# Performance work log

Hardware: AMD Instinct MI355X
Metric: run time of the kernel (lower is better)

The kernel has to match this reference:

```python
import jax, jax.numpy as jnp
import numpy as np

N_NODES = 100000
N_EDGES = 1600000
IN_FEATS = 128
OUT_FEATS = 128


def setup_inputs() -> dict:
    key = jax.random.key(0)
    ks = jax.random.split(key, 8)
    feat = jax.random.normal(ks[0], (N_NODES, IN_FEATS), dtype=jnp.float32)
    weight = jax.random.normal(ks[1], (IN_FEATS, OUT_FEATS), dtype=jnp.float32) * (1.0 / np.sqrt(IN_FEATS))
    bias = jnp.zeros((OUT_FEATS,), dtype=jnp.float32)
    s = 1.0 / np.sqrt(OUT_FEATS)
    w_ih = jax.random.uniform(ks[2], (3 * OUT_FEATS, IN_FEATS), dtype=jnp.float32, minval=-s, maxval=s)
    w_hh = jax.random.uniform(ks[3], (3 * OUT_FEATS, OUT_FEATS), dtype=jnp.float32, minval=-s, maxval=s)
    b_ih = jax.random.uniform(ks[4], (3 * OUT_FEATS,), dtype=jnp.float32, minval=-s, maxval=s)
    b_hh = jax.random.uniform(ks[5], (3 * OUT_FEATS,), dtype=jnp.float32, minval=-s, maxval=s)
    src = jax.random.randint(ks[6], (N_EDGES,), 0, N_NODES, dtype=jnp.int32)
    dst = jax.random.randint(ks[7], (N_EDGES,), 0, N_NODES, dtype=jnp.int32)
    return {"feat": feat, "weight": weight, "bias": bias,
            "w_ih": w_ih, "w_hh": w_hh, "b_ih": b_ih, "b_hh": b_hh,
            "src": src, "dst": dst}


def reference(feat, weight, bias, w_ih, w_hh, b_ih, b_hh, src, dst):
    n = feat.shape[0]
    # symmetric-ish GCN norm: in-degree^{-1/2}, clamped at 1
    deg = jax.ops.segment_sum(jnp.ones(dst.shape, feat.dtype), dst, num_segments=n)
    norm = jnp.power(jnp.clip(deg, 1.0, None), -0.5)[:, None]  # [N,1]
    featn = feat * norm
    # copy_src + sum aggregation (SpMM via gather + segment_sum), then matmul
    agg = jax.ops.segment_sum(featn[src], dst, num_segments=n)  # [N, in]
    rst = agg @ weight                                           # [N, out]
    rst = rst * norm + bias
    # GRUCell(input=featn, hidden=rst)
    gi = featn @ w_ih.T + b_ih   # [N, 3*out]
    gh = rst @ w_hh.T + b_hh     # [N, 3*out]
    i_r, i_z, i_n = jnp.split(gi, 3, axis=1)
    h_r, h_z, h_n = jnp.split(gh, 3, axis=1)
    r = jax.nn.sigmoid(i_r + h_r)
    z = jax.nn.sigmoid(i_z + h_z)
    nn_ = jnp.tanh(i_n + r * h_n)
    return (1.0 - z) * nn_ + z * rst
```

## Files before the change

### kernel.cpp

```cpp
#include <hip/hip_runtime.h>
#include <hip/hip_bf16.h>
#include <math.h>

#define N_NODES 100000
#define N_EDGES 1600000
#define F 128


#define WS_FEATN_OFF 8001536
#define WS_WTI_OFF   59201536
#define WS_WTH_OFF   59398144
#define WS_NEED_FULL (WS_WTH_OFF + 196608)

__global__ __launch_bounds__(256) void k_degree(const int* __restrict__ dst,
                                                int* __restrict__ deg) {
    int i = blockIdx.x * 256 + threadIdx.x;
    if (i < N_EDGES) atomicAdd(&deg[dst[i]], 1);
}

#define SCAN_B 512
#define SCAN_NB 196

__global__ __launch_bounds__(SCAN_B) void k_scan1(const int* __restrict__ deg,
                                                  int* __restrict__ bsum) {
    __shared__ int s[SCAN_B];
    int t = threadIdx.x;
    int i = blockIdx.x * SCAN_B + t;
    s[t] = (i < N_NODES) ? deg[i] : 0;
    __syncthreads();
    for (int o = SCAN_B / 2; o > 0; o >>= 1) {
        if (t < o) s[t] += s[t + o];
        __syncthreads();
    }
    if (t == 0) bsum[blockIdx.x] = s[0];
}

__global__ __launch_bounds__(256) void k_scan2(int* __restrict__ bsum) {
    __shared__ int s[256];
    int t = threadIdx.x;
    int v = (t < SCAN_NB) ? bsum[t] : 0;
    s[t] = v;
    __syncthreads();
    for (int o = 1; o < 256; o <<= 1) {
        int x = (t >= o) ? s[t - o] : 0;
        __syncthreads();
        s[t] += x;
        __syncthreads();
    }
    if (t < SCAN_NB) bsum[t] = (t == 0) ? 0 : s[t - 1];
}

__global__ __launch_bounds__(SCAN_B) void k_scan3(const int* __restrict__ deg,
                                                  const int* __restrict__ bsum,
                                                  int* __restrict__ offs,
                                                  float* __restrict__ norm) {
    __shared__ int s[SCAN_B];
    int t = threadIdx.x;
    int i = blockIdx.x * SCAN_B + t;
    int v = (i < N_NODES) ? deg[i] : 0;
    s[t] = v;
    __syncthreads();
    for (int o = 1; o < SCAN_B; o <<= 1) {
        int x = (t >= o) ? s[t - o] : 0;
        __syncthreads();
        s[t] += x;
        __syncthreads();
    }
    if (i < N_NODES) {
        offs[i] = bsum[blockIdx.x] + s[t] - v;
        norm[i] = rsqrtf(fmaxf((float)v, 1.0f));
    }
    if (blockIdx.x == 0 && t == 0) offs[N_NODES] = N_EDGES;
}

__global__ __launch_bounds__(256) void k_fill(const int* __restrict__ src,
                                              const int* __restrict__ dst,
                                              const int* __restrict__ offs,
                                              int* __restrict__ cursor,
                                              int* __restrict__ ssrc) {
    int i = blockIdx.x * 256 + threadIdx.x;
    if (i < N_EDGES) {
        int d = dst[i];
        int p = atomicAdd(&cursor[d], 1);
        ssrc[offs[d] + p] = src[i];
    }
}

__global__ __launch_bounds__(256) void k_featn(const float* __restrict__ feat,
                                               const float* __restrict__ norm,
                                               float* __restrict__ featn) {
    int idx = blockIdx.x * 256 + threadIdx.x;
    int row = idx >> 5;
    float nv = norm[row];
    float4 v = ((const float4*)feat)[idx];
    v.x *= nv; v.y *= nv; v.z *= nv; v.w *= nv;
    ((float4*)featn)[idx] = v;
}

__global__ __launch_bounds__(256) void k_wt(const float* __restrict__ w,
                                            float* __restrict__ wT) {
    __shared__ float tile[32][33];
    int rt = blockIdx.x >> 2, ct = blockIdx.x & 3;
    int r0 = rt * 32, c0 = ct * 32;
    int tr = threadIdx.x >> 5, tc = threadIdx.x & 31;
#pragma unroll
    for (int i = 0; i < 32; i += 8)
        tile[tr + i][tc] = w[(r0 + tr + i) * 128 + c0 + tc];
    __syncthreads();
#pragma unroll
    for (int i = 0; i < 32; i += 8)
        wT[(c0 + tr + i) * 384 + r0 + tc] = tile[tc][tr + i];
}

#define ROWS 16
template <bool PRE>
__global__ __launch_bounds__(256) void k_fused(
    const float* __restrict__ fsrc, const float* __restrict__ norm,
    const int* __restrict__ offs, const int* __restrict__ ssrc,
    const float* __restrict__ W, const float* __restrict__ bias,
    const float* __restrict__ wih_, const float* __restrict__ whh_,
    const float* __restrict__ b_ih, const float* __restrict__ b_hh,
    float* __restrict__ out) {
    __shared__ float sagg[ROWS][F];
    __shared__ float sfeat[ROWS][F];
    __shared__ float srst[ROWS][F];
    __shared__ float snorm[ROWS];

    int t = threadIdx.x;
    int row0 = blockIdx.x * ROWS;

    if (t < ROWS) snorm[t] = norm[row0 + t];
    for (int i = t; i < ROWS * (F / 4); i += 256) {
        int r = i >> 5, c = i & 31;
        float4 f = ((const float4*)(fsrc + (size_t)(row0 + r) * F))[c];
        if (!PRE) {
            float nv = norm[row0 + r];
            f.x *= nv; f.y *= nv; f.z *= nv; f.w *= nv;
        }
        ((float4*)&sfeat[r][0])[c] = f;
    }

    int wave = t >> 6, lane = t & 63;
    int hf = lane >> 5, sub = lane & 31;
    for (int ln = wave; ln < ROWS; ln += 4) {
        int node = row0 + ln;
        int beg = offs[node], end = offs[node + 1];
        float4 acc = make_float4(0.f, 0.f, 0.f, 0.f);
        int e = beg;
        for (; e + 7 < end; e += 8) {
            int s0 = ssrc[e + 0 + hf];
            int s1 = ssrc[e + 2 + hf];
            int s2 = ssrc[e + 4 + hf];
            int s3 = ssrc[e + 6 + hf];
            float4 v0 = *(const float4*)(fsrc + (size_t)s0 * F + sub * 4);
            float4 v1 = *(const float4*)(fsrc + (size_t)s1 * F + sub * 4);
            float4 v2 = *(const float4*)(fsrc + (size_t)s2 * F + sub * 4);
            float4 v3 = *(const float4*)(fsrc + (size_t)s3 * F + sub * 4);
            if (PRE) {
                acc.x += (v0.x + v1.x) + (v2.x + v3.x);
                acc.y += (v0.y + v1.y) + (v2.y + v3.y);
                acc.z += (v0.z + v1.z) + (v2.z + v3.z);
                acc.w += (v0.w + v1.w) + (v2.w + v3.w);
            } else {
                float n0 = norm[s0], n1 = norm[s1], n2 = norm[s2], n3 = norm[s3];
                acc.x = fmaf(v0.x, n0, acc.x); acc.y = fmaf(v0.y, n0, acc.y);
                acc.z = fmaf(v0.z, n0, acc.z); acc.w = fmaf(v0.w, n0, acc.w);
                acc.x = fmaf(v1.x, n1, acc.x); acc.y = fmaf(v1.y, n1, acc.y);
                acc.z = fmaf(v1.z, n1, acc.z); acc.w = fmaf(v1.w, n1, acc.w);
                acc.x = fmaf(v2.x, n2, acc.x); acc.y = fmaf(v2.y, n2, acc.y);
                acc.z = fmaf(v2.z, n2, acc.z); acc.w = fmaf(v2.w, n2, acc.w);
                acc.x = fmaf(v3.x, n3, acc.x); acc.y = fmaf(v3.y, n3, acc.y);
                acc.z = fmaf(v3.z, n3, acc.z); acc.w = fmaf(v3.w, n3, acc.w);
            }
        }
        for (; e < end; e += 2) {
            int edge = e + hf;
            if (edge < end) {
                int s0 = ssrc[edge];
                float4 v0 = *(const float4*)(fsrc + (size_t)s0 * F + sub * 4);
                float n0 = PRE ? 1.0f : norm[s0];
                acc.x = fmaf(v0.x, n0, acc.x); acc.y = fmaf(v0.y, n0, acc.y);
                acc.z = fmaf(v0.z, n0, acc.z); acc.w = fmaf(v0.w, n0, acc.w);
            }
        }
        acc.x += __shfl_xor(acc.x, 32, 64);
        acc.y += __shfl_xor(acc.y, 32, 64);
        acc.z += __shfl_xor(acc.z, 32, 64);
        acc.w += __shfl_xor(acc.w, 32, 64);
        if (hf == 0) *(float4*)&sagg[ln][sub * 4] = acc;
    }
    __syncthreads();

    int j = t & 127;
    int rg = (t >> 7) * 8;
    {
        float acc[8] = {0, 0, 0, 0, 0, 0, 0, 0};
        for (int k = 0; k < F; k += 4) {
            float w0 = W[(k + 0) * F + j];
            float w1 = W[(k + 1) * F + j];
            float w2 = W[(k + 2) * F + j];
            float w3 = W[(k + 3) * F + j];
#pragma unroll
            for (int r = 0; r < 8; ++r) {
                float4 a = *(const float4*)&sagg[rg + r][k];
                acc[r] = fmaf(a.x, w0, acc[r]);
                acc[r] = fmaf(a.y, w1, acc[r]);
                acc[r] = fmaf(a.z, w2, acc[r]);
                acc[r] = fmaf(a.w, w3, acc[r]);
            }
        }
        float bj = bias[j];
#pragma unroll
        for (int r = 0; r < 8; ++r) {
            srst[rg + r][j] = acc[r] * snorm[rg + r] + bj;
        }
    }
    __syncthreads();

    float air[8] = {0}, aiz[8] = {0}, ain[8] = {0};
    float ahr[8] = {0}, ahz[8] = {0}, ahn[8] = {0};

    if (PRE) {
        for (int k = 0; k < F; k += 4) {
            float wi[3][4], wh[3][4];
#pragma unroll
            for (int kk = 0; kk < 4; ++kk) {
                const float* wik = wih_ + (size_t)(k + kk) * 384 + j;
                const float* whk = whh_ + (size_t)(k + kk) * 384 + j;
                wi[0][kk] = wik[0];   wi[1][kk] = wik[128]; wi[2][kk] = wik[256];
                wh[0][kk] = whk[0];   wh[1][kk] = whk[128]; wh[2][kk] = whk[256];
            }
#pragma unroll
            for (int r = 0; r < 8; ++r) {
                float4 a = *(const float4*)&sfeat[rg + r][k];
                float4 h = *(const float4*)&srst[rg + r][k];
                air[r] = fmaf(a.x, wi[0][0], air[r]); air[r] = fmaf(a.y, wi[0][1], air[r]);
                air[r] = fmaf(a.z, wi[0][2], air[r]); air[r] = fmaf(a.w, wi[0][3], air[r]);
                aiz[r] = fmaf(a.x, wi[1][0], aiz[r]); aiz[r] = fmaf(a.y, wi[1][1], aiz[r]);
                aiz[r] = fmaf(a.z, wi[1][2], aiz[r]); aiz[r] = fmaf(a.w, wi[1][3], aiz[r]);
                ain[r] = fmaf(a.x, wi[2][0], ain[r]); ain[r] = fmaf(a.y, wi[2][1], ain[r]);
                ain[r] = fmaf(a.z, wi[2][2], ain[r]); ain[r] = fmaf(a.w, wi[2][3], ain[r]);
                ahr[r] = fmaf(h.x, wh[0][0], ahr[r]); ahr[r] = fmaf(h.y, wh[0][1], ahr[r]);
                ahr[r] = fmaf(h.z, wh[0][2], ahr[r]); ahr[r] = fmaf(h.w, wh[0][3], ahr[r]);
                ahz[r] = fmaf(h.x, wh[1][0], ahz[r]); ahz[r] = fmaf(h.y, wh[1][1], ahz[r]);
                ahz[r] = fmaf(h.z, wh[1][2], ahz[r]); ahz[r] = fmaf(h.w, wh[1][3], ahz[r]);
                ahn[r] = fmaf(h.x, wh[2][0], ahn[r]); ahn[r] = fmaf(h.y, wh[2][1], ahn[r]);
                ahn[r] = fmaf(h.z, wh[2][2], ahn[r]); ahn[r] = fmaf(h.w, wh[2][3], ahn[r]);
            }
        }
    } else {
        const float* wir = wih_ + (size_t)(j + 0) * F;
        const float* wiz = wih_ + (size_t)(j + 128) * F;
        const float* win = wih_ + (size_t)(j + 256) * F;
        const float* whr = whh_ + (size_t)(j + 0) * F;
        const float* whz = whh_ + (size_t)(j + 128) * F;
        const float* whn = whh_ + (size_t)(j + 256) * F;
        for (int k = 0; k < F; k += 4) {
            float4 bir = *(const float4*)(wir + k);
            float4 biz = *(const float4*)(wiz + k);
            float4 bin = *(const float4*)(win + k);
            float4 bhr = *(const float4*)(whr + k);
            float4 bhz = *(const float4*)(whz + k);
            float4 bhn = *(const float4*)(whn + k);
#pragma unroll
            for (int r = 0; r < 8; ++r) {
                float4 a = *(const float4*)&sfeat[rg + r][k];
                float4 h = *(const float4*)&srst[rg + r][k];
                air[r] = fmaf(a.x, bir.x, air[r]); air[r] = fmaf(a.y, bir.y, air[r]);
                air[r] = fmaf(a.z, bir.z, air[r]); air[r] = fmaf(a.w, bir.w, air[r]);
                aiz[r] = fmaf(a.x, biz.x, aiz[r]); aiz[r] = fmaf(a.y, biz.y, aiz[r]);
                aiz[r] = fmaf(a.z, biz.z, aiz[r]); aiz[r] = fmaf(a.w, biz.w, aiz[r]);
                ain[r] = fmaf(a.x, bin.x, ain[r]); ain[r] = fmaf(a.y, bin.y, ain[r]);
                ain[r] = fmaf(a.z, bin.z, ain[r]); ain[r] = fmaf(a.w, bin.w, ain[r]);
                ahr[r] = fmaf(h.x, bhr.x, ahr[r]); ahr[r] = fmaf(h.y, bhr.y, ahr[r]);
                ahr[r] = fmaf(h.z, bhr.z, ahr[r]); ahr[r] = fmaf(h.w, bhr.w, ahr[r]);
                ahz[r] = fmaf(h.x, bhz.x, ahz[r]); ahz[r] = fmaf(h.y, bhz.y, ahz[r]);
                ahz[r] = fmaf(h.z, bhz.z, ahz[r]); ahz[r] = fmaf(h.w, bhz.w, ahz[r]);
                ahn[r] = fmaf(h.x, bhn.x, ahn[r]); ahn[r] = fmaf(h.y, bhn.y, ahn[r]);
                ahn[r] = fmaf(h.z, bhn.z, ahn[r]); ahn[r] = fmaf(h.w, bhn.w, ahn[r]);
            }
        }
    }

    float Bir = b_ih[j], Biz = b_ih[j + 128], Bin = b_ih[j + 256];
    float Bhr = b_hh[j], Bhz = b_hh[j + 128], Bhn = b_hh[j + 256];
#pragma unroll
    for (int r = 0; r < 8; ++r) {
        int row = row0 + rg + r;
        float ir = air[r] + Bir, hr = ahr[r] + Bhr;
        float iz = aiz[r] + Biz, hz = ahz[r] + Bhz;
        float in_ = ain[r] + Bin, hn = ahn[r] + Bhn;
        float rr = 1.0f / (1.0f + __expf(-(ir + hr)));
        float zz = 1.0f / (1.0f + __expf(-(iz + hz)));
        float nn = tanhf(in_ + rr * hn);
        float rstv = srst[rg + r][j];
        out[(size_t)row * F + j] = (1.0f - zz) * nn + zz * rstv;
    }
}

extern "C" void kernel_launch(void* const* d_in, const int* in_sizes, int n_in,
                              void* d_out, int out_size, void* d_ws, size_t ws_size,
                              hipStream_t stream) {
    const float* feat   = (const float*)d_in[0];
    const float* weight = (const float*)d_in[1];
    const float* bias   = (const float*)d_in[2];
    const float* w_ih   = (const float*)d_in[3];
    const float* w_hh   = (const float*)d_in[4];
    const float* b_ih   = (const float*)d_in[5];
    const float* b_hh   = (const float*)d_in[6];
    const int*   src    = (const int*)d_in[7];
    const int*   dst    = (const int*)d_in[8];
    float* out = (float*)d_out;

    char* ws = (char*)d_ws;
    int*   deg    = (int*)(ws + 0);
    float* norm   = (float*)(ws + 400000);
    int*   offs   = (int*)(ws + 800000);
    int*   cursor = (int*)(ws + 1200016);
    int*   ssrc   = (int*)(ws + 1600016);
    int*   bsum   = (int*)(ws + 8000016);
    float* featn  = (float*)(ws + WS_FEATN_OFF);
    float* wT_ih  = (float*)(ws + WS_WTI_OFF);
    float* wT_hh  = (float*)(ws + WS_WTH_OFF);

    hipMemsetAsync(deg, 0, N_NODES * sizeof(int), stream);
    hipMemsetAsync(cursor, 0, N_NODES * sizeof(int), stream);

    k_degree<<<(N_EDGES + 255) / 256, 256, 0, stream>>>(dst, deg);
    k_scan1<<<SCAN_NB, SCAN_B, 0, stream>>>(deg, bsum);
    k_scan2<<<1, 256, 0, stream>>>(bsum);
    k_scan3<<<SCAN_NB, SCAN_B, 0, stream>>>(deg, bsum, offs, norm);
    k_fill<<<(N_EDGES + 255) / 256, 256, 0, stream>>>(src, dst, offs, cursor, ssrc);

    if (ws_size >= WS_NEED_FULL) {
        k_wt<<<48, 256, 0, stream>>>(w_ih, wT_ih);
        k_wt<<<48, 256, 0, stream>>>(w_hh, wT_hh);
        k_featn<<<(N_NODES * F / 4) / 256, 256, 0, stream>>>(feat, norm, featn);
        k_fused<true><<<N_NODES / ROWS, 256, 0, stream>>>(featn, norm, offs, ssrc,
                                                          weight, bias, wT_ih, wT_hh,
                                                          b_ih, b_hh, out);
    } else {
        k_fused<false><<<N_NODES / ROWS, 256, 0, stream>>>(feat, norm, offs, ssrc,
                                                           weight, bias, w_ih, w_hh,
                                                           b_ih, b_hh, out);
    }
}
```

Measured before the change: 738.1 us.

## Halve fused-kernel row tile, merge GRU accumulators, fold launches and memset

Halves the rows per block in the fused aggregation+GRU kernel from 16 to 8 and adds a launch-bounds occupancy hint. It also merges the r/z input and hidden accumulators so 4 accumulator arrays are kept instead of 6 and bias loads are folded. The goal is lower register pressure and more resident waves for the latency-bound gather. Separately, the cursor memset moves into the scan kernel and the two weight-transpose launches become one, cutting launch overhead. The cost is that each block now reloads W and the GRU weights for half as many rows, doubling weight traffic from cache per output row.

New measurement: 830.6 us. 1.13x slower.

```diff
diff --git a/kernel.cpp b/kernel.cpp
--- a/kernel.cpp
+++ b/kernel.cpp
@@ -53,7 +53,8 @@
 __global__ __launch_bounds__(SCAN_B) void k_scan3(const int* __restrict__ deg,
                                                   const int* __restrict__ bsum,
                                                   int* __restrict__ offs,
-                                                  float* __restrict__ norm) {
+                                                  float* __restrict__ norm,
+                                                  int* __restrict__ cursor) {
     __shared__ int s[SCAN_B];
     int t = threadIdx.x;
     int i = blockIdx.x * SCAN_B + t;
@@ -69,6 +70,7 @@
     if (i < N_NODES) {
         offs[i] = bsum[blockIdx.x] + s[t] - v;
         norm[i] = rsqrtf(fmaxf((float)v, 1.0f));
+        cursor[i] = 0;
     }
     if (blockIdx.x == 0 && t == 0) offs[N_NODES] = N_EDGES;
 }
@@ -97,10 +99,16 @@
     ((float4*)featn)[idx] = v;
 }
 
-__global__ __launch_bounds__(256) void k_wt(const float* __restrict__ w,
-                                            float* __restrict__ wT) {
+__global__ __launch_bounds__(256) void k_wt(const float* __restrict__ w_ih,
+                                            const float* __restrict__ w_hh,
+                                            float* __restrict__ wT_ih,
+                                            float* __restrict__ wT_hh) {
     __shared__ float tile[32][33];
-    int rt = blockIdx.x >> 2, ct = blockIdx.x & 3;
+    int b = blockIdx.x;
+    const float* w = (b < 48) ? w_ih : w_hh;
+    float* wT      = (b < 48) ? wT_ih : wT_hh;
+    int bb = (b < 48) ? b : b - 48;
+    int rt = bb >> 2, ct = bb & 3;
     int r0 = rt * 32, c0 = ct * 32;
     int tr = threadIdx.x >> 5, tc = threadIdx.x & 31;
 #pragma unroll
@@ -112,9 +120,9 @@
         wT[(c0 + tr + i) * 384 + r0 + tc] = tile[tc][tr + i];
 }
 
-#define ROWS 16
+#define ROWS 8
 template <bool PRE>
-__global__ __launch_bounds__(256) void k_fused(
+__global__ __launch_bounds__(256, 4) void k_fused(
     const float* __restrict__ fsrc, const float* __restrict__ norm,
     const int* __restrict__ offs, const int* __restrict__ ssrc,
     const float* __restrict__ W, const float* __restrict__ bias,
@@ -130,8 +138,8 @@
     int row0 = blockIdx.x * ROWS;
 
     if (t < ROWS) snorm[t] = norm[row0 + t];
-    for (int i = t; i < ROWS * (F / 4); i += 256) {
-        int r = i >> 5, c = i & 31;
+    {
+        int r = t >> 5, c = t & 31;
         float4 f = ((const float4*)(fsrc + (size_t)(row0 + r) * F))[c];
         if (!PRE) {
             float nv = norm[row0 + r];
@@ -192,16 +200,16 @@
     __syncthreads();
 
     int j = t & 127;
-    int rg = (t >> 7) * 8;
+    int rg = (t >> 7) * 4;
     {
-        float acc[8] = {0, 0, 0, 0, 0, 0, 0, 0};
+        float acc[4] = {0, 0, 0, 0};
         for (int k = 0; k < F; k += 4) {
             float w0 = W[(k + 0) * F + j];
             float w1 = W[(k + 1) * F + j];
             float w2 = W[(k + 2) * F + j];
             float w3 = W[(k + 3) * F + j];
 #pragma unroll
-            for (int r = 0; r < 8; ++r) {
+            for (int r = 0; r < 4; ++r) {
                 float4 a = *(const float4*)&sagg[rg + r][k];
                 acc[r] = fmaf(a.x, w0, acc[r]);
                 acc[r] = fmaf(a.y, w1, acc[r]);
@@ -211,88 +219,88 @@
         }
         float bj = bias[j];
 #pragma unroll
-        for (int r = 0; r < 8; ++r) {
+        for (int r = 0; r < 4; ++r) {
             srst[rg + r][j] = acc[r] * snorm[rg + r] + bj;
         }
     }
     __syncthreads();
 
-    float air[8] = {0}, aiz[8] = {0}, ain[8] = {0};
-    float ahr[8] = {0}, ahz[8] = {0}, ahn[8] = {0};
+    float accr[4] = {0, 0, 0, 0};
+    float accz[4] = {0, 0, 0, 0};
+    float accin[4] = {0, 0, 0, 0};
+    float acchn[4] = {0, 0, 0, 0};
 
     if (PRE) {
         for (int k = 0; k < F; k += 4) {
-            float wi[3][4], wh[3][4];
+            float wir[4], wiz[4], win[4], whr[4], whz[4], whn[4];
 #pragma unroll
             for (int kk = 0; kk < 4; ++kk) {
                 const float* wik = wih_ + (size_t)(k + kk) * 384 + j;
                 const float* whk = whh_ + (size_t)(k + kk) * 384 + j;
-                wi[0][kk] = wik[0];   wi[1][kk] = wik[128]; wi[2][kk] = wik[256];
-                wh[0][kk] = whk[0];   wh[1][kk] = whk[128]; wh[2][kk] = whk[256];
-            }
-#pragma unroll
-            for (int r = 0; r < 8; ++r) {
+                wir[kk] = wik[0]; wiz[kk] = wik[128]; win[kk] = wik[256];
+                whr[kk] = whk[0]; whz[kk] = whk[128]; whn[kk] = whk[256];
+            }
+#pragma unroll
+            for (int r = 0; r < 4; ++r) {
                 float4 a = *(const float4*)&sfeat[rg + r][k];
                 float4 h = *(const float4*)&srst[rg + r][k];
-                air[r] = fmaf(a.x, wi[0][0], air[r]); air[r] = fmaf(a.y, wi[0][1], air[r]);
-                air[r] = fmaf(a.z, wi[0][2], air[r]); air[r] = fmaf(a.w, wi[0][3], air[r]);
-                aiz[r] = fmaf(a.x, wi[1][0], aiz[r]); aiz[r] = fmaf(a.y, wi[1][1], aiz[r]);
-                aiz[r] = fmaf(a.z, wi[1][2], aiz[r]); aiz[r] = fmaf(a.w, wi[1][3], aiz[r]);
-                ain[r] = fmaf(a.x, wi[2][0], ain[r]); ain[r] = fmaf(a.y, wi[2][1], ain[r]);
-                ain[r] = fmaf(a.z, wi[2][2], ain[r]); ain[r] = fmaf(a.w, wi[2][3], ain[r]);
-                ahr[r] = fmaf(h.x, wh[0][0], ahr[r]); ahr[r] = fmaf(h.y, wh[0][1], ahr[r]);
-                ahr[r] = fmaf(h.z, wh[0][2], ahr[r]); ahr[r] = fmaf(h.w, wh[0][3], ahr[r]);
-                ahz[r] = fmaf(h.x, wh[1][0], ahz[r]); ahz[r] = fmaf(h.y, wh[1][1], ahz[r]);
-                ahz[r] = fmaf(h.z, wh[1][2], ahz[r]); ahz[r] = fmaf(h.w, wh[1][3], ahz[r]);
-                ahn[r] = fmaf(h.x, wh[2][0], ahn[r]); ahn[r] = fmaf(h.y, wh[2][1], ahn[r]);
-                ahn[r] = fmaf(h.z, wh[2][2], ahn[r]); ahn[r] = fmaf(h.w, wh[2][3], ahn[r]);
+                accr[r] = fmaf(a.x, wir[0], accr[r]); accr[r] = fmaf(h.x, whr[0], accr[r]);
+                accr[r] = fmaf(a.y, wir[1], accr[r]); accr[r] = fmaf(h.y, whr[1], accr[r]);
+                accr[r] = fmaf(a.z, wir[2], accr[r]); accr[r] = fmaf(h.z, whr[2], accr[r]);
+                accr[r] = fmaf(a.w, wir[3], accr[r]); accr[r] = fmaf(h.w, whr[3], accr[r]);
+                accz[r] = fmaf(a.x, wiz[0], accz[r]); accz[r] = fmaf(h.x, whz[0], accz[r]);
+                accz[r] = fmaf(a.y, wiz[1], accz[r]); accz[r] = fmaf(h.y, whz[1], accz[r]);
+                accz[r] = fmaf(a.z, wiz[2], accz[r]); accz[r] = fmaf(h.z, whz[2], accz[r]);
+                accz[r] = fmaf(a.w, wiz[3], accz[r]); accz[r] = fmaf(h.w, whz[3], accz[r]);
+                accin[r] = fmaf(a.x, win[0], accin[r]); accin[r] = fmaf(a.y, win[1], accin[r]);
+                accin[r] = fmaf(a.z, win[2], accin[r]); accin[r] = fmaf(a.w, win[3], accin[r]);
+                acchn[r] = fmaf(h.x, whn[0], acchn[r]); acchn[r] = fmaf(h.y, whn[1], acchn[r]);
+                acchn[r] = fmaf(h.z, whn[2], acchn[r]); acchn[r] = fmaf(h.w, whn[3], acchn[r]);
             }
         }
     } else {
-        const float* wir = wih_ + (size_t)(j + 0) * F;
-        const float* wiz = wih_ + (size_t)(j + 128) * F;
-        const float* win = wih_ + (size_t)(j + 256) * F;
-        const float* whr = whh_ + (size_t)(j + 0) * F;
-        const float* whz = whh_ + (size_t)(j + 128) * F;
-        const float* whn = whh_ + (size_t)(j + 256) * F;
+        const float* wirp = wih_ + (size_t)(j + 0) * F;
+        const float* wizp = wih_ + (size_t)(j + 128) * F;
+        const float* winp = wih_ + (size_t)(j + 256) * F;
+        const float* whrp = whh_ + (size_t)(j + 0) * F;
+        const float* whzp = whh_ + (size_t)(j + 128) * F;
+        const float* whnp = whh_ + (size_t)(j + 256) * F;
         for (int k = 0; k < F; k += 4) {
-            float4 bir = *(const float4*)(wir + k);
-            float4 biz = *(const float4*)(wiz + k);
-            float4 bin = *(const float4*)(win + k);
-            float4 bhr = *(const float4*)(whr + k);
-            float4 bhz = *(const float4*)(whz + k);
-            float4 bhn = *(const float4*)(whn + k);
-#pragma unroll
-            for (int r = 0; r < 8; ++r) {
+            float4 bir = *(const float4*)(wirp + k);
+            float4 biz = *(const float4*)(wizp + k);
+            float4 bin = *(const float4*)(winp + k);
+            float4 bhr = *(const float4*)(whrp + k);
+            float4 bhz = *(const float4*)(whzp + k);
+            float4 bhn = *(const float4*)(whnp + k);
+#pragma unroll
+            for (int r = 0; r < 4; ++r) {
                 float4 a = *(const float4*)&sfeat[rg + r][k];
                 float4 h = *(const float4*)&srst[rg + r][k];
-                air[r] = fmaf(a.x, bir.x, air[r]); air[r] = fmaf(a.y, bir.y, air[r]);
-                air[r] = fmaf(a.z, bir.z, air[r]); air[r] = fmaf(a.w, bir.w, air[r]);
-                aiz[r] = fmaf(a.x, biz.x, aiz[r]); aiz[r] = fmaf(a.y, biz.y, aiz[r]);
-                aiz[r] = fmaf(a.z, biz.z, aiz[r]); aiz[r] = fmaf(a.w, biz.w, aiz[r]);
-                ain[r] = fmaf(a.x, bin.x, ain[r]); ain[r] = fmaf(a.y, bin.y, ain[r]);
-                ain[r] = fmaf(a.z, bin.z, ain[r]); ain[r] = fmaf(a.w, bin.w, ain[r]);
-                ahr[r] = fmaf(h.x, bhr.x, ahr[r]); ahr[r] = fmaf(h.y, bhr.y, ahr[r]);
-                ahr[r] = fmaf(h.z, bhr.z, ahr[r]); ahr[r] = fmaf(h.w, bhr.w, ahr[r]);
-                ahz[r] = fmaf(h.x, bhz.x, ahz[r]); ahz[r] = fmaf(h.y, bhz.y, ahz[r]);
-                ahz[r] = fmaf(h.z, bhz.z, ahz[r]); ahz[r] = fmaf(h.w, bhz.w, ahz[r]);
-                ahn[r] = fmaf(h.x, bhn.x, ahn[r]); ahn[r] = fmaf(h.y, bhn.y, ahn[r]);
-                ahn[r] = fmaf(h.z, bhn.z, ahn[r]); ahn[r] = fmaf(h.w, bhn.w, ahn[r]);
-            }
-        }
-    }
-
-    float Bir = b_ih[j], Biz = b_ih[j + 128], Bin = b_ih[j + 256];
-    float Bhr = b_hh[j], Bhz = b_hh[j + 128], Bhn = b_hh[j + 256];
-#pragma unroll
-    for (int r = 0; r < 8; ++r) {
+                accr[r] = fmaf(a.x, bir.x, accr[r]); accr[r] = fmaf(h.x, bhr.x, accr[r]);
+                accr[r] = fmaf(a.y, bir.y, accr[r]); accr[r] = fmaf(h.y, bhr.y, accr[r]);
+                accr[r] = fmaf(a.z, bir.z, accr[r]); accr[r] = fmaf(h.z, bhr.z, accr[r]);
+                accr[r] = fmaf(a.w, bir.w, accr[r]); accr[r] = fmaf(h.w, bhr.w, accr[r]);
+                accz[r] = fmaf(a.x, biz.x, accz[r]); accz[r] = fmaf(h.x, bhz.x, accz[r]);
+                accz[r] = fmaf(a.y, biz.y, accz[r]); accz[r] = fmaf(h.y, bhz.y, accz[r]);
+                accz[r] = fmaf(a.z, biz.z, accz[r]); accz[r] = fmaf(h.z, bhz.z, accz[r]);
+                accz[r] = fmaf(a.w, biz.w, accz[r]); accz[r] = fmaf(h.w, bhz.w, accz[r]);
+                accin[r] = fmaf(a.x, bin.x, accin[r]); accin[r] = fmaf(a.y, bin.y, accin[r]);
+                accin[r] = fmaf(a.z, bin.z, accin[r]); accin[r] = fmaf(a.w, bin.w, accin[r]);
+                acchn[r] = fmaf(h.x, bhn.x, acchn[r]); acchn[r] = fmaf(h.y, bhn.y, acchn[r]);
+                acchn[r] = fmaf(h.z, bhn.z, acchn[r]); acchn[r] = fmaf(h.w, bhn.w, acchn[r]);
+            }
+        }
+    }
+
+    float Brz = b_ih[j] + b_hh[j];
+    float Bzz = b_ih[j + 128] + b_hh[j + 128];
+    float Bin = b_ih[j + 256], Bhn = b_hh[j + 256];
+#pragma unroll
+    for (int r = 0; r < 4; ++r) {
         int row = row0 + rg + r;
-        float ir = air[r] + Bir, hr = ahr[r] + Bhr;
-        float iz = aiz[r] + Biz, hz = ahz[r] + Bhz;
-        float in_ = ain[r] + Bin, hn = ahn[r] + Bhn;
-        float rr = 1.0f / (1.0f + __expf(-(ir + hr)));
-        float zz = 1.0f / (1.0f + __expf(-(iz + hz)));
-        float nn = tanhf(in_ + rr * hn);
+        float rr = 1.0f / (1.0f + __expf(-(accr[r] + Brz)));
+        float zz = 1.0f / (1.0f + __expf(-(accz[r] + Bzz)));
+        float nn = tanhf(accin[r] + Bin + rr * (acchn[r] + Bhn));
         float rstv = srst[rg + r][j];
         out[(size_t)row * F + j] = (1.0f - zz) * nn + zz * rstv;
     }
@@ -324,17 +332,15 @@
     float* wT_hh  = (float*)(ws + WS_WTH_OFF);
 
     hipMemsetAsync(deg, 0, N_NODES * sizeof(int), stream);
-    hipMemsetAsync(cursor, 0, N_NODES * sizeof(int), stream);
 
     k_degree<<<(N_EDGES + 255) / 256, 256, 0, stream>>>(dst, deg);
     k_scan1<<<SCAN_NB, SCAN_B, 0, stream>>>(deg, bsum);
     k_scan2<<<1, 256, 0, stream>>>(bsum);
-    k_scan3<<<SCAN_NB, SCAN_B, 0, stream>>>(deg, bsum, offs, norm);
+    k_scan3<<<SCAN_NB, SCAN_B, 0, stream>>>(deg, bsum, offs, norm, cursor);
     k_fill<<<(N_EDGES + 255) / 256, 256, 0, stream>>>(src, dst, offs, cursor, ssrc);
 
     if (ws_size >= WS_NEED_FULL) {
-        k_wt<<<48, 256, 0, stream>>>(w_ih, wT_ih);
-        k_wt<<<48, 256, 0, stream>>>(w_hh, wT_hh);
+        k_wt<<<96, 256, 0, stream>>>(w_ih, w_hh, wT_ih, wT_hh);
         k_featn<<<(N_NODES * F / 4) / 256, 256, 0, stream>>>(feat, norm, featn);
         k_fused<true><<<N_NODES / ROWS, 256, 0, stream>>>(featn, norm, offs, ssrc,
                                                           weight, bias, wT_ih, wT_hh,
```
